# Kernel tuning notes

Hardware: AMD Instinct MI355X
Metric: run time of the kernel (lower is better)

Reference implementation:

```python
import jax, jax.numpy as jnp
import numpy as np

EMB = 768
HEADS = 12
HEAD_DIM = EMB // HEADS
SEQ = 4096
BATCH = 1


def setup_inputs() -> dict:
    key = jax.random.key(0)
    ks = jax.random.split(key, 9)
    s = 1.0 / np.sqrt(EMB)
    return {
        "x": jax.random.normal(ks[0], (BATCH, SEQ, EMB), dtype=jnp.float32),
        "wq": jax.random.normal(ks[1], (EMB, EMB), dtype=jnp.float32) * s,
        "bq": jax.random.normal(ks[2], (EMB,), dtype=jnp.float32) * s,
        "wk": jax.random.normal(ks[3], (EMB, EMB), dtype=jnp.float32) * s,
        "bk": jax.random.normal(ks[4], (EMB,), dtype=jnp.float32) * s,
        "wv": jax.random.normal(ks[5], (EMB, EMB), dtype=jnp.float32) * s,
        "bv": jax.random.normal(ks[6], (EMB,), dtype=jnp.float32) * s,
        "wo": jax.random.normal(ks[7], (EMB, EMB), dtype=jnp.float32) * s,
        "bo": jax.random.normal(ks[8], (EMB,), dtype=jnp.float32) * s,
    }


def reference(x, wq, bq, wk, bk, wv, bv, wo, bo):
    b, n, _ = x.shape
    # projections: [b, n, emb] -> [b, heads, n, head_dim]
    def split_heads(t):
        return t.reshape(b, n, HEADS, HEAD_DIM).transpose(0, 2, 1, 3)
    q = split_heads(x @ wq + bq)
    k = split_heads(x @ wk + bk)
    v = split_heads(x @ wv + bv)
    # full N x N scores (naive attention, as in the original)
    scores = jnp.einsum("bhqd,bhkd->bhqk", q, k)
    causal = jnp.triu(jnp.ones((n, n), dtype=bool), k=1)
    scores = jnp.where(causal, -jnp.inf, scores)
    weights = jax.nn.softmax(scores / np.sqrt(HEAD_DIM), axis=-1)
    # dropout with rate 0.0 is identity (eval mode)
    ctx = jnp.einsum("bhqk,bhkd->bhqd", weights, v)
    ctx = ctx.transpose(0, 2, 1, 3).reshape(b, n, EMB)
    return ctx @ wo + bo
```

## Files before the change

kernel.cpp:

```cpp
#include <hip/hip_runtime.h>
#include <stdint.h>

#define SEQ 4096
#define EMB 768
#define HEADS 12
#define HD 64
#define NQT (SEQ / 64)

typedef __attribute__((ext_vector_type(8))) short short8;
typedef __attribute__((ext_vector_type(4))) short short4v;
typedef __attribute__((ext_vector_type(8))) __bf16 bf16x8;
typedef __attribute__((ext_vector_type(4))) __bf16 bf16x4;
typedef __attribute__((ext_vector_type(4))) float f32x4;

#define QSCALE 0.18033688011112043f

static __device__ __forceinline__ unsigned short f2bf(float f) {
    unsigned int u = __builtin_bit_cast(unsigned int, f);
    unsigned int r = 0x7fffu + ((u >> 16) & 1u);
    u += r;
    return (unsigned short)(u >> 16);
}

static __device__ __forceinline__ f32x4 mfma32(short8 a, short8 b, f32x4 c) {
    return __builtin_amdgcn_mfma_f32_16x16x32_bf16(
        __builtin_bit_cast(bf16x8, a), __builtin_bit_cast(bf16x8, b), c, 0, 0, 0);
}

static __device__ __forceinline__ f32x4 mfma16(short4v a, short4v b, f32x4 c) {
#if __has_builtin(__builtin_amdgcn_mfma_f32_16x16x16_bf16)
    return __builtin_amdgcn_mfma_f32_16x16x16_bf16(
        __builtin_bit_cast(bf16x4, a), __builtin_bit_cast(bf16x4, b), c, 0, 0, 0);
#else
    return __builtin_amdgcn_mfma_f32_16x16x16bf16_1k(a, b, c, 0, 0, 0);
#endif
}

static __device__ __forceinline__ short4v pack4bf(float a, float b, float c, float d) {
#if __has_builtin(__builtin_amdgcn_cvt_pk_bf16_f32)
    typedef __attribute__((ext_vector_type(2))) __bf16 bf16x2;
    bf16x2 lo = __builtin_amdgcn_cvt_pk_bf16_f32(a, b);
    bf16x2 hi = __builtin_amdgcn_cvt_pk_bf16_f32(c, d);
    uint2 u = {__builtin_bit_cast(unsigned int, lo), __builtin_bit_cast(unsigned int, hi)};
    return __builtin_bit_cast(short4v, u);
#else
    short4v p;
    p[0] = (short)f2bf(a); p[1] = (short)f2bf(b);
    p[2] = (short)f2bf(c); p[3] = (short)f2bf(d);
    return p;
#endif
}

static __device__ __forceinline__ void load_lds16(const void* g, void* l) {
    __builtin_amdgcn_global_load_lds(
        (const __attribute__((address_space(1))) unsigned int*)(uintptr_t)g,
        (__attribute__((address_space(3))) unsigned int*)(uintptr_t)l, 16, 0, 0);
}

__global__ __launch_bounds__(256) void convert_all(const float* __restrict__ x,
                                                   const float* __restrict__ wq,
                                                   const float* __restrict__ wk,
                                                   const float* __restrict__ wv,
                                                   const float* __restrict__ wo,
                                                   unsigned short* __restrict__ xb,
                                                   unsigned short* __restrict__ wqkvT,
                                                   unsigned short* __restrict__ woT) {
    __shared__ float Ls[64][65];
    const int bid = blockIdx.x;
    if (bid < 3072) {
        int i = bid * 256 + threadIdx.x;
        float4 v = ((const float4*)x)[i];
        ushort4 o = {f2bf(v.x), f2bf(v.y), f2bf(v.z), f2bf(v.w)};
        ((ushort4*)xb)[i] = o;
        return;
    }
    const int idx = bid - 3072;
    const int z = idx / 144;
    const int bx = (idx % 144) / 12, by = idx % 12;
    const float* W = (z == 0) ? wq : (z == 1) ? wk : (z == 2) ? wv : wo;
    unsigned short* dst = (z < 3) ? (wqkvT + (size_t)z * EMB * EMB) : woT;
    const int k0 = bx * 64, n0 = by * 64;
    const int r = threadIdx.x >> 2, c0 = (threadIdx.x & 3) * 16;
    for (int j = 0; j < 16; j += 4) {
        float4 v = *(const float4*)&W[(size_t)(k0 + r) * EMB + n0 + c0 + j];
        Ls[r][c0 + j] = v.x;
        Ls[r][c0 + j + 1] = v.y;
        Ls[r][c0 + j + 2] = v.z;
        Ls[r][c0 + j + 3] = v.w;
    }
    __syncthreads();
    unsigned short tmp[16];
    for (int j = 0; j < 16; j++) tmp[j] = f2bf(Ls[c0 + j][r]);
    *(uint4*)&dst[(size_t)(n0 + r) * EMB + k0 + c0] = *(uint4*)tmp;
    *(uint4*)&dst[(size_t)(n0 + r) * EMB + k0 + c0 + 8] = *(uint4*)(tmp + 8);
}

__global__ __launch_bounds__(256) void gemm_qkv(const unsigned short* __restrict__ A,
                                                const unsigned short* __restrict__ Bt,
                                                const float* __restrict__ b0p,
                                                const float* __restrict__ b1p,
                                                const float* __restrict__ b2p,
                                                unsigned short* __restrict__ QKb,
                                                unsigned short* __restrict__ Vtb) {
    __shared__ __align__(16) unsigned short As[128 * 32];
    __shared__ __align__(16) unsigned short Bs[128 * 32];
    const int tid = threadIdx.x;
    const int wave = tid >> 6, lane = tid & 63, quad = lane >> 4, l16 = lane & 15;
    const int m0 = blockIdx.x * 128, n0 = blockIdx.y * 128;
    const int wm = (wave >> 1) * 64, wn = (wave & 1) * 64;
    const int lrow = lane >> 2, lcol = (lane & 3) * 8;

    f32x4 acc[4][4] = {};

    for (int k0 = 0; k0 < EMB; k0 += 32) {
        __syncthreads();
        for (int t = 0; t < 2; t++) {
            int row = wave * 32 + t * 16 + lrow;
            load_lds16(&A[(size_t)(m0 + row) * EMB + k0 + lcol], &As[(wave * 2 + t) * 512]);
            load_lds16(&Bt[(size_t)(n0 + row) * EMB + k0 + lcol], &Bs[(wave * 2 + t) * 512]);
        }
        __syncthreads();
        short8 a[4], b[4];
        for (int i = 0; i < 4; i++) a[i] = *(const short8*)&As[(wm + i * 16 + l16) * 32 + quad * 8];
        for (int i = 0; i < 4; i++) b[i] = *(const short8*)&Bs[(wn + i * 16 + l16) * 32 + quad * 8];
        for (int i = 0; i < 4; i++)
            for (int j = 0; j < 4; j++) acc[i][j] = mfma32(a[i], b[j], acc[i][j]);
    }

    const int z = n0 / EMB;
    if (z < 2) {
        const float* bias = z ? b1p : b0p;
        const float sc = z ? 1.0f : QSCALE;
        for (int i = 0; i < 4; i++)
            for (int j = 0; j < 4; j++) {
                int mbase = m0 + wm + i * 16 + quad * 4;
                int n = n0 + wn + j * 16 + l16;
                float bv = bias[n - z * EMB];
                for (int r = 0; r < 4; r++)
                    QKb[(size_t)(mbase + r) * 1536 + n] = f2bf((acc[i][j][r] + bv) * sc);
            }
    } else {
        for (int i = 0; i < 4; i++)
            for (int j = 0; j < 4; j++) {
                int mbase = m0 + wm + i * 16 + quad * 4;
                int nn = n0 + wn + j * 16 + l16 - 2 * EMB;
                int h = nn >> 6, d = nn & 63;
                float bv = b2p[nn];
                ushort4 pk;
                pk.x = f2bf(acc[i][j][0] + bv);
                pk.y = f2bf(acc[i][j][1] + bv);
                pk.z = f2bf(acc[i][j][2] + bv);
                pk.w = f2bf(acc[i][j][3] + bv);
                *(ushort4*)&Vtb[(size_t)(h * HD + d) * SEQ + mbase] = pk;
            }
    }
}

__global__ __launch_bounds__(256) void gemm_out(const unsigned short* __restrict__ A,
                                                const unsigned short* __restrict__ Bt,
                                                const float* __restrict__ bias,
                                                float* __restrict__ outp) {
    __shared__ __align__(16) unsigned short As[64 * 32];
    __shared__ __align__(16) unsigned short Bs[128 * 32];
    const int tid = threadIdx.x;
    const int wave = tid >> 6, lane = tid & 63, quad = lane >> 4, l16 = lane & 15;
    const int m0 = blockIdx.x * 64, n0 = blockIdx.y * 128;
    const int wm = (wave >> 1) * 32, wn = (wave & 1) * 64;
    const int lrow = lane >> 2, lcol = (lane & 3) * 8;

    f32x4 acc[2][4] = {};

    for (int k0 = 0; k0 < EMB; k0 += 32) {
        __syncthreads();
        load_lds16(&A[(size_t)(m0 + wave * 16 + lrow) * EMB + k0 + lcol], &As[wave * 512]);
        for (int t = 0; t < 2; t++) {
            int row = wave * 32 + t * 16 + lrow;
            load_lds16(&Bt[(size_t)(n0 + row) * EMB + k0 + lcol], &Bs[(wave * 2 + t) * 512]);
        }
        __syncthreads();
        short8 a[2], b[4];
        for (int i = 0; i < 2; i++) a[i] = *(const short8*)&As[(wm + i * 16 + l16) * 32 + quad * 8];
        for (int j = 0; j < 4; j++) b[j] = *(const short8*)&Bs[(wn + j * 16 + l16) * 32 + quad * 8];
        for (int i = 0; i < 2; i++)
            for (int j = 0; j < 4; j++) acc[i][j] = mfma32(a[i], b[j], acc[i][j]);
    }

    for (int i = 0; i < 2; i++)
        for (int j = 0; j < 4; j++) {
            int mbase = m0 + wm + i * 16 + quad * 4;
            int n = n0 + wn + j * 16 + l16;
            float bv = bias[n];
            for (int r = 0; r < 4; r++) outp[(size_t)(mbase + r) * EMB + n] = acc[i][j][r] + bv;
        }
}

__global__ __launch_bounds__(256) void attn_kernel(const unsigned short* __restrict__ QKb,
                                                   const unsigned short* __restrict__ Vtb,
                                                   unsigned short* __restrict__ ctxb,
                                                   unsigned short* __restrict__ Op,
                                                   float* __restrict__ mArr,
                                                   float* __restrict__ lArr) {
    __shared__ __align__(16) unsigned short Ks[64 * 64];
    __shared__ __align__(16) unsigned short Vs[64 * 64];

    const int bid = blockIdx.x;
    const int h = bid / 120;
    const int rem = bid % 120;
    int qt, ch, nch;
    if (rem < 24) {
        qt = rem; ch = 0; nch = 1;
    } else if (rem < 72) {
        int q2 = rem - 24;
        qt = 24 + (q2 >> 1); ch = q2 & 1; nch = 2;
    } else {
        int q3 = rem - 72;
        qt = 48 + q3 / 3; ch = q3 % 3; nch = 3;
    }
    const int kb = (ch * (qt + 1)) / nch;
    const int ke = ((ch + 1) * (qt + 1)) / nch - 1;
    const int qbase = qt * 64;
    const int tid = threadIdx.x;
    const int wave = tid >> 6, lane = tid & 63, quad = lane >> 4, l16 = lane & 15;

    const unsigned short* Qg = QKb + (size_t)h * HD;
    const unsigned short* Kg = QKb + (size_t)(EMB + h * HD);
    const unsigned short* Vh = Vtb + (size_t)h * HD * SEQ;

    const int q = qbase + wave * 16 + l16;
    const short8 bQ0 = *(const short8*)&Qg[(size_t)q * 1536 + quad * 8];
    const short8 bQ1 = *(const short8*)&Qg[(size_t)q * 1536 + 32 + quad * 8];

    const int row = tid >> 2, t4 = tid & 3, cg = t4 * 16;
    const int swk = row & 7, swv = row & 15;

    f32x4 O[4] = {};
    float m_i = -3.0e38f, l_i = 0.f;

    uint4 kr0, kr1, vr0, vr1;
    {
        const int kb64 = kb * 64;
        kr0 = *(const uint4*)&Kg[(size_t)(kb64 + row) * 1536 + cg];
        kr1 = *(const uint4*)&Kg[(size_t)(kb64 + row) * 1536 + cg + 8];
        vr0 = *(const uint4*)&Vh[(size_t)row * SEQ + kb64 + cg];
        vr1 = *(const uint4*)&Vh[(size_t)row * SEQ + kb64 + cg + 8];
    }

    for (int kt = kb; kt <= ke; kt++) {
        const int kbase = kt * 64;
        __syncthreads();
        *(uint4*)&Ks[row * 64 + ((2 * t4) ^ swk) * 8] = kr0;
        *(uint4*)&Ks[row * 64 + ((2 * t4 + 1) ^ swk) * 8] = kr1;
        *(uint2*)&Vs[row * 64 + ((4 * t4) ^ swv) * 4] = ((const uint2*)&vr0)[0];
        *(uint2*)&Vs[row * 64 + ((4 * t4 + 1) ^ swv) * 4] = ((const uint2*)&vr0)[1];
        *(uint2*)&Vs[row * 64 + ((4 * t4 + 2) ^ swv) * 4] = ((const uint2*)&vr1)[0];
        *(uint2*)&Vs[row * 64 + ((4 * t4 + 3) ^ swv) * 4] = ((const uint2*)&vr1)[1];
        if (kt < ke) {
            const int nb = kbase + 64;
            kr0 = *(const uint4*)&Kg[(size_t)(nb + row) * 1536 + cg];
            kr1 = *(const uint4*)&Kg[(size_t)(nb + row) * 1536 + cg + 8];
            vr0 = *(const uint4*)&Vh[(size_t)row * SEQ + nb + cg];
            vr1 = *(const uint4*)&Vh[(size_t)row * SEQ + nb + cg + 8];
        }
        __syncthreads();

        const int swr = l16 & 7;
        f32x4 st[4];
        for (int nt = 0; nt < 4; nt++) {
            short8 aK0 = *(const short8*)&Ks[(nt * 16 + l16) * 64 + (quad ^ swr) * 8];
            short8 aK1 = *(const short8*)&Ks[(nt * 16 + l16) * 64 + ((quad + 4) ^ swr) * 8];
            f32x4 z = {};
            z = mfma32(aK0, bQ0, z);
            z = mfma32(aK1, bQ1, z);
            st[nt] = z;
        }
        if (kt == qt) {
            for (int nt = 0; nt < 4; nt++)
                for (int r = 0; r < 4; r++)
                    if (kbase + nt * 16 + quad * 4 + r > q) st[nt][r] = -INFINITY;
        }
        float mx = -3.0e38f;
        for (int nt = 0; nt < 4; nt++)
            for (int r = 0; r < 4; r++) mx = fmaxf(mx, st[nt][r]);
        mx = fmaxf(mx, __shfl_xor(mx, 16));
        mx = fmaxf(mx, __shfl_xor(mx, 32));
        const bool inc = mx > m_i;
        if (__ballot(inc)) {
            const float mn = inc ? mx : m_i;
            const float alpha = __builtin_amdgcn_exp2f(m_i - mn);
            m_i = mn;
            l_i *= alpha;
            for (int dt = 0; dt < 4; dt++)
                for (int r = 0; r < 4; r++) O[dt][r] *= alpha;
        }
        float rs = 0.f;
        short4v pk[4];
        for (int nt = 0; nt < 4; nt++) {
            float p0 = __builtin_amdgcn_exp2f(st[nt][0] - m_i);
            float p1 = __builtin_amdgcn_exp2f(st[nt][1] - m_i);
            float p2 = __builtin_amdgcn_exp2f(st[nt][2] - m_i);
            float p3 = __builtin_amdgcn_exp2f(st[nt][3] - m_i);
            rs += p0 + p1 + p2 + p3;
            pk[nt] = pack4bf(p0, p1, p2, p3);
        }
        rs += __shfl_xor(rs, 16);
        rs += __shfl_xor(rs, 32);
        l_i += rs;
        for (int dt = 0; dt < 4; dt++)
            for (int nt = 0; nt < 4; nt++) {
                short4v av = *(const short4v*)&Vs[(dt * 16 + l16) * 64 + ((4 * nt + quad) ^ l16) * 4];
                O[dt] = mfma16(av, pk[nt], O[dt]);
            }
    }

    const int ql = wave * 16 + l16;
    if (nch == 1) {
        const float inv = 1.f / l_i;
        for (int dt = 0; dt < 4; dt++) {
            ushort4 o;
            o.x = f2bf(O[dt][0] * inv);
            o.y = f2bf(O[dt][1] * inv);
            o.z = f2bf(O[dt][2] * inv);
            o.w = f2bf(O[dt][3] * inv);
            *(ushort4*)&ctxb[(size_t)q * EMB + h * HD + dt * 16 + quad * 4] = o;
        }
    } else {
        if (ch == 0) {
            for (int dt = 0; dt < 4; dt++) {
                ushort4 o;
                o.x = f2bf(O[dt][0]);
                o.y = f2bf(O[dt][1]);
                o.z = f2bf(O[dt][2]);
                o.w = f2bf(O[dt][3]);
                *(ushort4*)&ctxb[(size_t)q * EMB + h * HD + dt * 16 + quad * 4] = o;
            }
        } else {
            const int pid = (qt < 48) ? h * 56 + (qt - 24)
                                      : h * 56 + 24 + (qt - 48) * 2 + (ch - 1);
            for (int dt = 0; dt < 4; dt++) {
                ushort4 o;
                o.x = f2bf(O[dt][0]);
                o.y = f2bf(O[dt][1]);
                o.z = f2bf(O[dt][2]);
                o.w = f2bf(O[dt][3]);
                *(ushort4*)&Op[(size_t)pid * 4096 + ql * 64 + dt * 16 + quad * 4] = o;
            }
        }
        if (quad == 0) {
            const int mli = ((h * 64 + qt) * 3 + ch) * 64 + ql;
            mArr[mli] = m_i;
            lArr[mli] = l_i;
        }
    }
}

__global__ __launch_bounds__(256) void merge_kernel(const unsigned short* __restrict__ Op,
                                                    const float* __restrict__ mArr,
                                                    const float* __restrict__ lArr,
                                                    unsigned short* __restrict__ ctxb) {
    const int gid = blockIdx.x;
    const int h = gid / 40;
    const int qt = 24 + gid % 40;
    const int nch = qt / 24 + 1;
    const int q = threadIdx.x >> 2, d0 = (threadIdx.x & 3) * 16;
    const int mlbase = (h * 64 + qt) * 3;

    float mc[3], lc[3];
    for (int c = 0; c < nch; c++) {
        mc[c] = mArr[(mlbase + c) * 64 + q];
        lc[c] = lArr[(mlbase + c) * 64 + q];
    }
    float M = mc[0];
    for (int c = 1; c < nch; c++) M = fmaxf(M, mc[c]);
    float w[3], L = 0.f;
    for (int c = 0; c < nch; c++) {
        w[c] = __builtin_amdgcn_exp2f(mc[c] - M);
        L += w[c] * lc[c];
    }
    const float inv = 1.f / L;
    for (int c = 0; c < nch; c++) w[c] *= inv;

    unsigned short* dst = &ctxb[(size_t)(qt * 64 + q) * EMB + h * HD + d0];
    for (int jj = 0; jj < 16; jj += 8) {
        uint4 u0 = *(const uint4*)&dst[jj];
        float f[8];
        const unsigned short* p0 = (const unsigned short*)&u0;
        for (int t = 0; t < 8; t++)
            f[t] = w[0] * __builtin_bit_cast(float, (unsigned int)p0[t] << 16);
        for (int c = 1; c < nch; c++) {
            const int pid = (qt < 48) ? h * 56 + (qt - 24)
                                      : h * 56 + 24 + (qt - 48) * 2 + (c - 1);
            uint4 u = *(const uint4*)&Op[(size_t)pid * 4096 + q * 64 + d0 + jj];
            const unsigned short* p = (const unsigned short*)&u;
            for (int t = 0; t < 8; t++)
                f[t] += w[c] * __builtin_bit_cast(float, (unsigned int)p[t] << 16);
        }
        unsigned short o[8];
        for (int t = 0; t < 8; t++) o[t] = f2bf(f[t]);
        *(uint4*)&dst[jj] = *(uint4*)o;
    }
}

extern "C" void kernel_launch(void* const* d_in, const int* in_sizes, int n_in,
                              void* d_out, int out_size, void* d_ws, size_t ws_size,
                              hipStream_t stream) {
    const float* x = (const float*)d_in[0];
    const float* wq = (const float*)d_in[1];
    const float* bq = (const float*)d_in[2];
    const float* wk = (const float*)d_in[3];
    const float* bk = (const float*)d_in[4];
    const float* wv = (const float*)d_in[5];
    const float* bv = (const float*)d_in[6];
    const float* wo = (const float*)d_in[7];
    const float* bo = (const float*)d_in[8];

    unsigned short* ws = (unsigned short*)d_ws;
    unsigned short* xb = ws;
    unsigned short* wqkvT = xb + SEQ * EMB;
    unsigned short* woT = wqkvT + 3 * EMB * EMB;
    unsigned short* QKb = woT + EMB * EMB;
    unsigned short* Vtb = QKb + (size_t)SEQ * 1536;
    unsigned short* ctxb = Vtb + HEADS * SEQ * HD;
    unsigned short* Op = xb;
    float* mArr = (float*)wqkvT;
    float* lArr = mArr + 2304 * 64;

    convert_all<<<dim3(3072 + 576), 256, 0, stream>>>(x, wq, wk, wv, wo, xb, wqkvT, woT);
    gemm_qkv<<<dim3(SEQ / 128, 3 * EMB / 128), 256, 0, stream>>>(
        xb, wqkvT, bq, bk, bv, QKb, Vtb);
    attn_kernel<<<dim3(1440), 256, 0, stream>>>(QKb, Vtb, ctxb, Op, mArr, lArr);
    merge_kernel<<<dim3(480), 256, 0, stream>>>(Op, mArr, lArr, ctxb);
    gemm_out<<<dim3(SEQ / 64, EMB / 128), 256, 0, stream>>>(ctxb, woT, bo, (float*)d_out);
}
```

Before: 209.5 us.

## Rebalance causal attention split-K chunks, reverse block order, stage V transpose via LDS

Repartitions causal query tiles into four bands with up to four KV chunks each, and launches the heaviest work first by reversing block order, interleaving heads. The merge kernel and the partial-output indexing are updated to match the new chunk layout, and the m/l arrays move to a dedicated workspace region. The V-projection epilogue now transposes through shared memory so the writes to Vt are coalesced 16-byte row stores instead of scattered 8-byte stores. The aim is less tail imbalance and cheaper V stores, at the cost of more blocks, more merge traffic and extra barriers in the epilogue.

```diff
diff --git a/kernel.cpp b/kernel.cpp
--- a/kernel.cpp
+++ b/kernel.cpp
@@ -55,6 +55,11 @@
     __builtin_amdgcn_global_load_lds(
         (const __attribute__((address_space(1))) unsigned int*)(uintptr_t)g,
         (__attribute__((address_space(3))) unsigned int*)(uintptr_t)l, 16, 0, 0);
+}
+
+static __device__ __forceinline__ int pid_of(int h, int qt, int ch) {
+    int b = (qt < 40) ? (qt - 20) : (qt < 60 ? 20 + (qt - 40) * 2 : 60 + (qt - 60) * 3);
+    return h * 72 + b + (ch - 1);
 }
 
 __global__ __launch_bounds__(256) void convert_all(const float* __restrict__ x,
@@ -102,8 +107,9 @@
                                                 const float* __restrict__ b2p,
                                                 unsigned short* __restrict__ QKb,
                                                 unsigned short* __restrict__ Vtb) {
-    __shared__ __align__(16) unsigned short As[128 * 32];
-    __shared__ __align__(16) unsigned short Bs[128 * 32];
+    __shared__ __align__(16) unsigned short SMEM[8192];
+    unsigned short* As = SMEM;
+    unsigned short* Bs = SMEM + 4096;
     const int tid = threadIdx.x;
     const int wave = tid >> 6, lane = tid & 63, quad = lane >> 4, l16 = lane & 15;
     const int m0 = blockIdx.x * 128, n0 = blockIdx.y * 128;
@@ -140,19 +146,27 @@
                     QKb[(size_t)(mbase + r) * 1536 + n] = f2bf((acc[i][j][r] + bv) * sc);
             }
     } else {
-        for (int i = 0; i < 4; i++)
-            for (int j = 0; j < 4; j++) {
-                int mbase = m0 + wm + i * 16 + quad * 4;
-                int nn = n0 + wn + j * 16 + l16 - 2 * EMB;
-                int h = nn >> 6, d = nn & 63;
-                float bv = b2p[nn];
+        const int nn = n0 + wn + l16 - 2 * EMB;
+        for (int j = 0; j < 4; j++) {
+            __syncthreads();
+            const float bv = b2p[nn + j * 16];
+            const int nloc = (wave & 1) * 16 + l16;
+            for (int i = 0; i < 4; i++) {
                 ushort4 pk;
                 pk.x = f2bf(acc[i][j][0] + bv);
                 pk.y = f2bf(acc[i][j][1] + bv);
                 pk.z = f2bf(acc[i][j][2] + bv);
                 pk.w = f2bf(acc[i][j][3] + bv);
-                *(ushort4*)&Vtb[(size_t)(h * HD + d) * SEQ + mbase] = pk;
+                *(ushort4*)&SMEM[nloc * 136 + wm + i * 16 + quad * 4] = pk;
             }
+            __syncthreads();
+            const int nl = tid >> 3, c = tid & 7;
+            const int ng = (nl >> 4) * 64 + j * 16 + (nl & 15) + n0 + 0 * 0 - 2 * EMB;
+            const int hh = ng >> 6, dd = ng & 63;
+            unsigned short* dst = &Vtb[(size_t)(hh * HD + dd) * SEQ + m0];
+            *(uint4*)&dst[c * 8] = *(uint4*)&SMEM[nl * 136 + c * 8];
+            *(uint4*)&dst[64 + c * 8] = *(uint4*)&SMEM[nl * 136 + 64 + c * 8];
+        }
     }
 }
 
@@ -204,20 +218,20 @@
     __shared__ __align__(16) unsigned short Vs[64 * 64];
 
     const int bid = blockIdx.x;
-    const int h = bid / 120;
-    const int rem = bid % 120;
+    const int h = bid % HEADS;
+    const int rem = 135 - bid / HEADS;
     int qt, ch, nch;
-    if (rem < 24) {
+    if (rem < 20) {
         qt = rem; ch = 0; nch = 1;
-    } else if (rem < 72) {
-        int q2 = rem - 24;
-        qt = 24 + (q2 >> 1); ch = q2 & 1; nch = 2;
+    } else if (rem < 60) {
+        int t = rem - 20; qt = 20 + (t >> 1); ch = t & 1; nch = 2;
+    } else if (rem < 120) {
+        int t = rem - 60; qt = 40 + t / 3; ch = t % 3; nch = 3;
     } else {
-        int q3 = rem - 72;
-        qt = 48 + q3 / 3; ch = q3 % 3; nch = 3;
-    }
-    const int kb = (ch * (qt + 1)) / nch;
-    const int ke = ((ch + 1) * (qt + 1)) / nch - 1;
+        int t = rem - 120; qt = 60 + (t >> 2); ch = t & 3; nch = 4;
+    }
+    const int kb = ch * (qt + 1) / nch;
+    const int ke = (ch + 1) * (qt + 1) / nch - 1;
     const int qbase = qt * 64;
     const int tid = threadIdx.x;
     const int wave = tid >> 6, lane = tid & 63, quad = lane >> 4, l16 = lane & 15;
@@ -334,8 +348,7 @@
                 *(ushort4*)&ctxb[(size_t)q * EMB + h * HD + dt * 16 + quad * 4] = o;
             }
         } else {
-            const int pid = (qt < 48) ? h * 56 + (qt - 24)
-                                      : h * 56 + 24 + (qt - 48) * 2 + (ch - 1);
+            const int pid = pid_of(h, qt, ch);
             for (int dt = 0; dt < 4; dt++) {
                 ushort4 o;
                 o.x = f2bf(O[dt][0]);
@@ -346,7 +359,7 @@
             }
         }
         if (quad == 0) {
-            const int mli = ((h * 64 + qt) * 3 + ch) * 64 + ql;
+            const int mli = ((h * 64 + qt) * 4 + ch) * 64 + ql;
             mArr[mli] = m_i;
             lArr[mli] = l_i;
         }
@@ -358,20 +371,20 @@
                                                     const float* __restrict__ lArr,
                                                     unsigned short* __restrict__ ctxb) {
     const int gid = blockIdx.x;
-    const int h = gid / 40;
-    const int qt = 24 + gid % 40;
-    const int nch = qt / 24 + 1;
+    const int h = gid / 44;
+    const int qt = 20 + gid % 44;
+    const int nch = (qt < 40) ? 2 : (qt < 60) ? 3 : 4;
     const int q = threadIdx.x >> 2, d0 = (threadIdx.x & 3) * 16;
-    const int mlbase = (h * 64 + qt) * 3;
-
-    float mc[3], lc[3];
+    const int mlbase = (h * 64 + qt) * 4;
+
+    float mc[4], lc[4];
     for (int c = 0; c < nch; c++) {
         mc[c] = mArr[(mlbase + c) * 64 + q];
         lc[c] = lArr[(mlbase + c) * 64 + q];
     }
     float M = mc[0];
     for (int c = 1; c < nch; c++) M = fmaxf(M, mc[c]);
-    float w[3], L = 0.f;
+    float w[4], L = 0.f;
     for (int c = 0; c < nch; c++) {
         w[c] = __builtin_amdgcn_exp2f(mc[c] - M);
         L += w[c] * lc[c];
@@ -387,8 +400,7 @@
         for (int t = 0; t < 8; t++)
             f[t] = w[0] * __builtin_bit_cast(float, (unsigned int)p0[t] << 16);
         for (int c = 1; c < nch; c++) {
-            const int pid = (qt < 48) ? h * 56 + (qt - 24)
-                                      : h * 56 + 24 + (qt - 48) * 2 + (c - 1);
+            const int pid = pid_of(h, qt, c);
             uint4 u = *(const uint4*)&Op[(size_t)pid * 4096 + q * 64 + d0 + jj];
             const unsigned short* p = (const unsigned short*)&u;
             for (int t = 0; t < 8; t++)
@@ -421,13 +433,13 @@
     unsigned short* Vtb = QKb + (size_t)SEQ * 1536;
     unsigned short* ctxb = Vtb + HEADS * SEQ * HD;
     unsigned short* Op = xb;
-    float* mArr = (float*)wqkvT;
-    float* lArr = mArr + 2304 * 64;
+    float* mArr = (float*)(ws + 864 * 4096);
+    float* lArr = mArr + 12 * 64 * 4 * 64;
 
     convert_all<<<dim3(3072 + 576), 256, 0, stream>>>(x, wq, wk, wv, wo, xb, wqkvT, woT);
     gemm_qkv<<<dim3(SEQ / 128, 3 * EMB / 128), 256, 0, stream>>>(
         xb, wqkvT, bq, bk, bv, QKb, Vtb);
-    attn_kernel<<<dim3(1440), 256, 0, stream>>>(QKb, Vtb, ctxb, Op, mArr, lArr);
-    merge_kernel<<<dim3(480), 256, 0, stream>>>(Op, mArr, lArr, ctxb);
+    attn_kernel<<<dim3(12 * 136), 256, 0, stream>>>(QKb, Vtb, ctxb, Op, mArr, lArr);
+    merge_kernel<<<dim3(528), 256, 0, stream>>>(Op, mArr, lArr, ctxb);
     gemm_out<<<dim3(SEQ / 64, EMB / 128), 256, 0, stream>>>(ctxb, woT, bo, (float*)d_out);
 }
```

Result: faster. 205.3 us (-2.0%).
